# Performance work log

Hardware: AMD Instinct MI355X
Metric: run time of the kernel (lower is better)

The kernel has to match this reference:

```python
import jax, jax.numpy as jnp
import numpy as np

B, T, D = 4, 2048, 1024
GROUPS = 32
EPS = 1e-5
THETA = 10000.0


def _rope(x):
    # lucidrains RotaryEmbedding: interleaved pairs over the full dim
    d = x.shape[-1]
    t = x.shape[-2]
    inv_freq = 1.0 / (THETA ** (jnp.arange(0, d, 2, dtype=jnp.float32) / d))  # [d/2]
    freqs = jnp.arange(t, dtype=jnp.float32)[:, None] * inv_freq[None, :]      # [T, d/2]
    cos = jnp.cos(freqs).astype(x.dtype)
    sin = jnp.sin(freqs).astype(x.dtype)
    x1 = x[..., 0::2]
    x2 = x[..., 1::2]
    r1 = x1 * cos - x2 * sin
    r2 = x1 * sin + x2 * cos
    return jnp.stack([r1, r2], axis=-1).reshape(x.shape)


def _group_norm(z, weight, bias):
    # z: [N, C]; normalize per group of C//GROUPS channels
    n, c = z.shape
    zg = z.reshape(n, GROUPS, c // GROUPS)
    mean = zg.mean(axis=-1, keepdims=True)
    var = zg.var(axis=-1, keepdims=True)
    zg = (zg - mean) * jax.lax.rsqrt(var + EPS)
    return zg.reshape(n, c) * weight + bias


def setup_inputs() -> dict:
    key = jax.random.key(0)
    k1, k2, k3 = jax.random.split(key, 3)
    x = jax.random.normal(k1, (B, T, D), dtype=jnp.float32)
    W_in = jax.random.normal(k2, (D, 3 * D), dtype=jnp.float32) * (1.0 / np.sqrt(D))
    b_in = jax.random.normal(k3, (3 * D,), dtype=jnp.float32) * 0.02
    gn_weight = jnp.ones((D,), dtype=jnp.float32)
    gn_bias = jnp.zeros((D,), dtype=jnp.float32)
    return {"x": x, "W_in": W_in, "b_in": b_in, "gn_weight": gn_weight, "gn_bias": gn_bias}


def reference(x, W_in, b_in, gn_weight, gn_bias):
    b, t, c = x.shape
    qkv = x @ W_in + b_in                    # [B,T,3D]
    Q, K, V = jnp.split(qkv, 3, axis=-1)
    Q = jax.nn.relu(_rope(Q))
    K = jax.nn.relu(_rope(K))
    V = jax.nn.relu(V)
    A = jnp.einsum('btd,bsd->bts', Q, K)     # [B,T,T], no softmax
    y = jnp.einsum('bts,bsd->btd', A, V)     # [B,T,D]
    y = _group_norm(y.reshape(-1, c), gn_weight, gn_bias).reshape(b, t, c)
    # faithful to original: transpose(-2,-1).reshape(B,T,dim)
    return jnp.swapaxes(y, -2, -1).reshape(b, t, c)
```

## Files before the change

kernel.cpp:

```cpp
#include <hip/hip_runtime.h>


typedef unsigned short u16;
typedef __attribute__((ext_vector_type(8))) unsigned short u16x8;
typedef __attribute__((ext_vector_type(4))) float fx4;
typedef __attribute__((ext_vector_type(8))) __bf16 bfx8;

#define TP 129

__device__ __forceinline__ u16 f2bh(float v) {
  unsigned u = __float_as_uint(v);
  return (u16)((u + 0x7FFFu + ((u >> 16) & 1u)) >> 16);
}
__device__ __forceinline__ fx4 mfma16(bfx8 a, bfx8 b, fx4 c) {
  return __builtin_amdgcn_mfma_f32_16x16x32_bf16(a, b, c, 0, 0, 0);
}

__device__ __forceinline__ void gload16(const u16* g, u16* l) {
  __builtin_amdgcn_global_load_lds(
      (const __attribute__((address_space(1))) unsigned int*)(const void*)g,
      (__attribute__((address_space(3))) unsigned int*)(void*)l, 16, 0, 0);
}

__device__ __forceinline__ bfx8 ldsw(const u16* lds, int row, int slot) {
  const char* p = (const char*)lds + row * 128 + ((slot ^ (row & 7)) << 4);
  return __builtin_bit_cast(bfx8, *reinterpret_cast<const u16x8*>(p));
}

__device__ __forceinline__ void stage4(const u16* __restrict__ A,
                                       size_t rowBase, int stride, int k0,
                                       u16* lds, int w, int lane) {
#pragma unroll
  for (int i = 0; i < 4; ++i) {
    int c = ((w * 4 + i) << 6) + lane;
    int r = c >> 3, s = c & 7;
    int t = s ^ (r & 7);
    const u16* src = A + (rowBase + (size_t)r) * (size_t)stride + k0 + (t << 3);
    gload16(src, lds + ((w * 4 + i) << 9));
  }
}

__device__ inline void gemm_core_pipe(const u16* __restrict__ A, size_t aBase, int aStr,
                                      const u16* __restrict__ B, size_t bBase, int bStr, int K,
                                      u16* sA0, u16* sB0, u16* sA1, u16* sB1,
                                      fx4 acc[4][4], int w, int lane) {
  int wm = (w >> 1) * 64, wn = (w & 1) * 64;
  int lr = lane & 15, lk = lane >> 4;
  stage4(A, aBase, aStr, 0, sA0, w, lane);
  stage4(B, bBase, bStr, 0, sB0, w, lane);
  int NT = K >> 6;
  for (int t = 0; t < NT; ++t) {
    u16* cA = (t & 1) ? sA1 : sA0;
    u16* cB = (t & 1) ? sB1 : sB0;
    if (t + 1 < NT) {
      u16* nA = (t & 1) ? sA0 : sA1;
      u16* nB = (t & 1) ? sB0 : sB1;
      stage4(A, aBase, aStr, (t + 1) << 6, nA, w, lane);
      stage4(B, bBase, bStr, (t + 1) << 6, nB, w, lane);
      asm volatile("s_waitcnt vmcnt(8)" ::: "memory");
    } else {
      asm volatile("s_waitcnt vmcnt(0)" ::: "memory");
    }
    __builtin_amdgcn_s_barrier();
    __builtin_amdgcn_sched_barrier(0);
    bfx8 a[8], b[8];
#pragma unroll
    for (int h = 0; h < 2; ++h)
#pragma unroll
      for (int i = 0; i < 4; ++i) {
        a[h * 4 + i] = ldsw(cA, wm + i * 16 + lr, h * 4 + lk);
        b[h * 4 + i] = ldsw(cB, wn + i * 16 + lr, h * 4 + lk);
      }
    asm volatile("s_waitcnt lgkmcnt(0)" ::: "memory");
    __builtin_amdgcn_sched_barrier(0);
    __builtin_amdgcn_s_barrier();
#pragma unroll
    for (int h = 0; h < 2; ++h)
#pragma unroll
      for (int mi = 0; mi < 4; ++mi)
#pragma unroll
        for (int ni = 0; ni < 4; ++ni)
          acc[mi][ni] = mfma16(a[h * 4 + mi], b[h * 4 + ni], acc[mi][ni]);
  }
}

__global__ void k_ropetab(float2* __restrict__ tabTI, float2* __restrict__ tabIT) {
  int idx = blockIdx.x * 256 + threadIdx.x;
  int t, i;
  if (blockIdx.y == 0) {
    t = idx >> 9;
    i = idx & 511;
  } else {
    i = idx >> 11;
    t = idx & 2047;
  }
  float invf = exp2f(-(float)i * (13.287712379549449f / 512.f));
  float ang = (float)t * invf, s, c;
  sincosf(ang, &s, &c);
  if (blockIdx.y == 0)
    tabTI[idx] = make_float2(c, s);
  else
    tabIT[idx] = make_float2(c, s);
}

__global__ void k_transW(const float* __restrict__ W, u16* __restrict__ WTh) {
  __shared__ float tile[32][33];
  int n0 = blockIdx.x * 32, k0 = blockIdx.y * 32;
  int tid = threadIdx.x;
  int c = tid & 31, r4 = tid >> 5;
#pragma unroll
  for (int it = 0; it < 4; ++it) {
    int r = r4 + it * 8;
    tile[r][c] = W[(size_t)(k0 + r) * 3072 + n0 + c];
  }
  __syncthreads();
#pragma unroll
  for (int it = 0; it < 4; ++it) {
    int r = r4 + it * 8;
    WTh[(size_t)(n0 + r) * 1024 + k0 + c] = f2bh(tile[c][r]);
  }
}

__global__ void k_castX(const float* __restrict__ x, u16* __restrict__ xh) {
  size_t i = ((size_t)blockIdx.x * 256 + threadIdx.x) * 8;
  fx4 v0 = *reinterpret_cast<const fx4*>(x + i);
  fx4 v1 = *reinterpret_cast<const fx4*>(x + i + 4);
  u16x8 h;
#pragma unroll
  for (int j = 0; j < 4; ++j) {
    h[j] = f2bh(v0[j]);
    h[4 + j] = f2bh(v1[j]);
  }
  *reinterpret_cast<u16x8*>(xh + i) = h;
}

__global__ __launch_bounds__(256) void k_gemm1f(const u16* __restrict__ xh,
                                                const u16* __restrict__ WTh,
                                                const float* __restrict__ b_in,
                                                const float2* __restrict__ tabTI,
                                                const float2* __restrict__ tabIT,
                                                u16* __restrict__ Qh, u16* __restrict__ Kth,
                                                u16* __restrict__ Vth) {
  __shared__ __align__(16) float shbuf[128 * TP];
  u16* sA0 = (u16*)shbuf;
  u16* sB0 = sA0 + 128 * 64;
  u16* sA1 = sB0 + 128 * 64;
  u16* sB1 = sA1 + 128 * 64;
  int bid = blockIdx.x;
  int xcd = bid & 7, idx = bid >> 3;
  int mt = (xcd << 3) + (idx & 7), nt = idx >> 3;
  int m0 = mt << 7, n0 = nt << 7;
  int tid = threadIdx.x, lane = tid & 63, w = tid >> 6;
  int wm = (w >> 1) * 64, wn = (w & 1) * 64;
  int lr = lane & 15, lk = lane >> 4;
  fx4 acc[4][4];
#pragma unroll
  for (int i = 0; i < 4; ++i)
#pragma unroll
    for (int j = 0; j < 4; ++j) acc[i][j] = fx4{0.f, 0.f, 0.f, 0.f};

  gemm_core_pipe(xh, (size_t)m0, 1024, WTh, (size_t)n0, 1024, 1024,
                 sA0, sB0, sA1, sB1, acc, w, lane);

  float bv[4];
#pragma unroll
  for (int ni = 0; ni < 4; ++ni) bv[ni] = b_in[n0 + wn + ni * 16 + lr];
  __syncthreads();
#pragma unroll
  for (int mi = 0; mi < 4; ++mi)
#pragma unroll
    for (int ni = 0; ni < 4; ++ni)
#pragma unroll
      for (int r = 0; r < 4; ++r)
        shbuf[(wn + ni * 16 + lr) * TP + wm + mi * 16 + lk * 4 + r] = acc[mi][ni][r] + bv[ni];
  __syncthreads();

  int part = n0 >> 10;
  int d0 = n0 - (part << 10);
  int bb = m0 >> 11, tb = m0 & 2047;
  int rl0 = tid >> 4;
  int cc = (tid & 15) * 8;

  if (part == 2) {
#pragma unroll
    for (int pass = 0; pass < 8; ++pass) {
      int rl = rl0 + pass * 16;
      u16x8 o;
#pragma unroll
      for (int j = 0; j < 8; ++j) o[j] = f2bh(fmaxf(shbuf[rl * TP + cc + j], 0.f));
      *reinterpret_cast<u16x8*>(Vth + (((size_t)(bb << 10) + d0 + rl) << 11) + tb + cc) = o;
    }
  } else if (part == 1) {
#pragma unroll
    for (int pass = 0; pass < 8; ++pass) {
      int rl = rl0 + pass * 16;
      int d = d0 + rl;
      const float2* tp = tabIT + ((size_t)(d >> 1) << 11) + tb + cc;
      const float* e = shbuf + (rl & ~1) * TP + cc;
      const float* oo = shbuf + (rl | 1) * TP + cc;
      int isOdd = d & 1;
      u16x8 o;
#pragma unroll
      for (int j = 0; j < 8; ++j) {
        float2 cs = tp[j];
        float x1 = e[j], x2 = oo[j];
        float v = isOdd ? (x1 * cs.y + x2 * cs.x) : (x1 * cs.x - x2 * cs.y);
        o[j] = f2bh(fmaxf(v, 0.f));
      }
      *reinterpret_cast<u16x8*>(Kth + (((size_t)(bb << 10) + d) << 11) + tb + cc) = o;
    }
  } else {
#pragma unroll
    for (int pass = 0; pass < 8; ++pass) {
      int rl = rl0 + pass * 16;
      int m = m0 + rl, t = m & 2047;
      const float2* tp = tabTI + ((size_t)t << 9) + ((d0 + cc) >> 1);
      u16x8 o;
#pragma unroll
      for (int jp = 0; jp < 4; ++jp) {
        float x1 = shbuf[(cc + 2 * jp) * TP + rl];
        float x2 = shbuf[(cc + 2 * jp + 1) * TP + rl];
        float2 cs = tp[jp];
        o[2 * jp] = f2bh(fmaxf(x1 * cs.x - x2 * cs.y, 0.f));
        o[2 * jp + 1] = f2bh(fmaxf(x1 * cs.y + x2 * cs.x, 0.f));
      }
      *reinterpret_cast<u16x8*>(Qh + ((size_t)m << 10) + d0 + cc) = o;
    }
  }
}

__global__ __launch_bounds__(256) void k_gemm2(const u16* __restrict__ Kth, const u16* __restrict__ Vth,
                                               u16* __restrict__ KtVTh) {
  __shared__ u16 smem[4 * 128 * 64];
  u16* sA0 = smem;
  u16* sB0 = sA0 + 128 * 64;
  u16* sA1 = sB0 + 128 * 64;
  u16* sB1 = sA1 + 128 * 64;
  fx4 acc[4][4];
#pragma unroll
  for (int i = 0; i < 4; ++i)
#pragma unroll
    for (int j = 0; j < 4; ++j) acc[i][j] = fx4{0.f, 0.f, 0.f, 0.f};
  int b = blockIdx.z;
  int m0 = blockIdx.x << 7, n0 = blockIdx.y << 7;
  int tid = threadIdx.x, lane = tid & 63, w = tid >> 6;
  const u16* Ab = Kth + ((size_t)b << 21);
  const u16* Bb = Vth + ((size_t)b << 21);
  gemm_core_pipe(Ab, (size_t)m0, 2048, Bb, (size_t)n0, 2048, 2048,
                 sA0, sB0, sA1, sB1, acc, w, lane);
  int wm = (w >> 1) * 64, wn = (w & 1) * 64, lr = lane & 15, lk = lane >> 4;
#pragma unroll
  for (int mi = 0; mi < 4; ++mi)
#pragma unroll
    for (int ni = 0; ni < 4; ++ni)
#pragma unroll
      for (int r = 0; r < 4; ++r) {
        int m = m0 + wm + mi * 16 + lk * 4 + r;
        int n = n0 + wn + ni * 16 + lr;
        KtVTh[((size_t)b << 20) + ((size_t)n << 10) + m] = f2bh(acc[mi][ni][r]);
      }
}

__global__ __launch_bounds__(256) void k_gemm3g(const u16* __restrict__ Qh, const u16* __restrict__ KtVTh,
                                                const float* __restrict__ gw, const float* __restrict__ gb,
                                                float* __restrict__ out) {
  __shared__ u16 smem[4 * 128 * 64];
  u16* sA0 = smem;
  u16* sB0 = sA0 + 128 * 64;
  u16* sA1 = sB0 + 128 * 64;
  u16* sB1 = sA1 + 128 * 64;
  fx4 acc[4][4];
#pragma unroll
  for (int i = 0; i < 4; ++i)
#pragma unroll
    for (int j = 0; j < 4; ++j) acc[i][j] = fx4{0.f, 0.f, 0.f, 0.f};
  int b = blockIdx.z;
  int m0 = blockIdx.x << 7, n0 = blockIdx.y << 7;
  int tid = threadIdx.x, lane = tid & 63, w = tid >> 6;
  gemm_core_pipe(Qh, (size_t)(b * 2048 + m0), 1024, KtVTh + ((size_t)b << 20), (size_t)n0, 1024,
                 1024, sA0, sB0, sA1, sB1, acc, w, lane);
  int wm = (w >> 1) * 64, wn = (w & 1) * 64, lr = lane & 15, lk = lane >> 4;
  float wv[4], bvv[4];
#pragma unroll
  for (int ni = 0; ni < 4; ++ni) {
    int n = n0 + wn + ni * 16 + lr;
    wv[ni] = gw[n];
    bvv[ni] = gb[n];
  }
#pragma unroll
  for (int mi = 0; mi < 4; ++mi) {
    fx4 o0, o1, o2, o3;
#pragma unroll
    for (int r = 0; r < 4; ++r) {
      float v0 = acc[mi][0][r], v1 = acc[mi][1][r], v2 = acc[mi][2][r], v3 = acc[mi][3][r];
      float sA2 = v0 + v1, sB2 = v2 + v3;
#pragma unroll
      for (int mk = 1; mk <= 8; mk <<= 1) {
        sA2 += __shfl_xor(sA2, mk);
        sB2 += __shfl_xor(sB2, mk);
      }
      float mA = sA2 * (1.f / 32.f), mB = sB2 * (1.f / 32.f);
      float dA = (v0 - mA) * (v0 - mA) + (v1 - mA) * (v1 - mA);
      float dB = (v2 - mB) * (v2 - mB) + (v3 - mB) * (v3 - mB);
#pragma unroll
      for (int mk = 1; mk <= 8; mk <<= 1) {
        dA += __shfl_xor(dA, mk);
        dB += __shfl_xor(dB, mk);
      }
      float rA = rsqrtf(dA * (1.f / 32.f) + 1e-5f);
      float rB = rsqrtf(dB * (1.f / 32.f) + 1e-5f);
      o0[r] = (v0 - mA) * rA * wv[0] + bvv[0];
      o1[r] = (v1 - mA) * rA * wv[1] + bvv[1];
      o2[r] = (v2 - mB) * rB * wv[2] + bvv[2];
      o3[r] = (v3 - mB) * rB * wv[3] + bvv[3];
    }
    int mbase = m0 + wm + mi * 16 + lk * 4;
#pragma unroll
    for (int ni = 0; ni < 4; ++ni) {
      int n = n0 + wn + ni * 16 + lr;
      fx4 ov = (ni == 0) ? o0 : (ni == 1) ? o1 : (ni == 2) ? o2 : o3;
      *reinterpret_cast<fx4*>(out + (((size_t)(b << 10) + n) << 11) + mbase) = ov;
    }
  }
}

extern "C" void kernel_launch(void* const* d_in, const int* in_sizes, int n_in,
                              void* d_out, int out_size, void* d_ws, size_t ws_size,
                              hipStream_t stream) {
  const float* x = (const float*)d_in[0];
  const float* W = (const float*)d_in[1];
  const float* b_in = (const float*)d_in[2];
  const float* gnw = (const float*)d_in[3];
  const float* gnb = (const float*)d_in[4];
  float* out = (float*)d_out;
  char* ws = (char*)d_ws;

  u16* xh = (u16*)(ws + 0);
  u16* WTh = (u16*)(ws + 16777216);
  u16* Qh = (u16*)(ws + 23068672);
  u16* Kth = (u16*)(ws + 39845888);
  u16* Vth = (u16*)(ws + 56623104);
  u16* KtVTh = (u16*)(ws + 73400320);
  float2* tabTI = (float2*)(ws + 81788928);
  float2* tabIT = (float2*)(ws + 90177536);

  k_ropetab<<<dim3(4096, 2), 256, 0, stream>>>(tabTI, tabIT);
  k_transW<<<dim3(96, 32), 256, 0, stream>>>(W, WTh);
  k_castX<<<4096, 256, 0, stream>>>(x, xh);
  k_gemm1f<<<1536, 256, 0, stream>>>(xh, WTh, b_in, tabTI, tabIT, Qh, Kth, Vth);
  k_gemm2<<<dim3(8, 8, 4), 256, 0, stream>>>(Kth, Vth, KtVTh);
  k_gemm3g<<<dim3(16, 8, 4), 256, 0, stream>>>(Qh, KtVTh, gnw, gnb, out);
}
```

Baseline: 146.1 us.

## Switch GEMMs to 32x32x16 MFMA and merge prep kernels into one launch

Replaces the 16x16x32 bf16 MFMA tiles with 32x32x16 MFMA (2x2 f32x16 accumulators per wave) in all three GEMMs. The LDS fragment loads and every epilogue (bias/RoPE staging, KtV store, group-norm) are rewritten to match the new accumulator layout, with the KtV stores vectorised to 4-wide. The three preprocessing kernels (rope table, W transpose, x cast) are merged into one launch. The aim is fewer MFMA issues per K step, fewer LDS reads and less launch overhead. In exchange the group-norm reduction now needs more cross-lane shuffles.

Measured after the change: 155.0 us. +6.1%, slower.

```diff
diff --git a/kernel.cpp b/kernel.cpp
--- a/kernel.cpp
+++ b/kernel.cpp
@@ -2,8 +2,10 @@
 
 
 typedef unsigned short u16;
+typedef __attribute__((ext_vector_type(4))) unsigned short u16x4;
 typedef __attribute__((ext_vector_type(8))) unsigned short u16x8;
 typedef __attribute__((ext_vector_type(4))) float fx4;
+typedef __attribute__((ext_vector_type(16))) float f32x16;
 typedef __attribute__((ext_vector_type(8))) __bf16 bfx8;
 
 #define TP 129
@@ -12,8 +14,8 @@
   unsigned u = __float_as_uint(v);
   return (u16)((u + 0x7FFFu + ((u >> 16) & 1u)) >> 16);
 }
-__device__ __forceinline__ fx4 mfma16(bfx8 a, bfx8 b, fx4 c) {
-  return __builtin_amdgcn_mfma_f32_16x16x32_bf16(a, b, c, 0, 0, 0);
+__device__ __forceinline__ f32x16 mfma32(bfx8 a, bfx8 b, f32x16 c) {
+  return __builtin_amdgcn_mfma_f32_32x32x16_bf16(a, b, c, 0, 0, 0);
 }
 
 __device__ __forceinline__ void gload16(const u16* g, u16* l) {
@@ -43,9 +45,9 @@
 __device__ inline void gemm_core_pipe(const u16* __restrict__ A, size_t aBase, int aStr,
                                       const u16* __restrict__ B, size_t bBase, int bStr, int K,
                                       u16* sA0, u16* sB0, u16* sA1, u16* sB1,
-                                      fx4 acc[4][4], int w, int lane) {
+                                      f32x16 acc[2][2], int w, int lane) {
   int wm = (w >> 1) * 64, wn = (w & 1) * 64;
-  int lr = lane & 15, lk = lane >> 4;
+  int ln = lane & 31, hi = lane >> 5;
   stage4(A, aBase, aStr, 0, sA0, w, lane);
   stage4(B, bBase, bStr, 0, sB0, w, lane);
   int NT = K >> 6;
@@ -63,75 +65,77 @@
     }
     __builtin_amdgcn_s_barrier();
     __builtin_amdgcn_sched_barrier(0);
-    bfx8 a[8], b[8];
-#pragma unroll
-    for (int h = 0; h < 2; ++h)
-#pragma unroll
-      for (int i = 0; i < 4; ++i) {
-        a[h * 4 + i] = ldsw(cA, wm + i * 16 + lr, h * 4 + lk);
-        b[h * 4 + i] = ldsw(cB, wn + i * 16 + lr, h * 4 + lk);
+    bfx8 a[2][4], b[2][4];
+#pragma unroll
+    for (int rb = 0; rb < 2; ++rb)
+#pragma unroll
+      for (int ks = 0; ks < 4; ++ks) {
+        a[rb][ks] = ldsw(cA, wm + rb * 32 + ln, ks * 2 + hi);
+        b[rb][ks] = ldsw(cB, wn + rb * 32 + ln, ks * 2 + hi);
       }
     asm volatile("s_waitcnt lgkmcnt(0)" ::: "memory");
     __builtin_amdgcn_sched_barrier(0);
     __builtin_amdgcn_s_barrier();
 #pragma unroll
-    for (int h = 0; h < 2; ++h)
-#pragma unroll
-      for (int mi = 0; mi < 4; ++mi)
-#pragma unroll
-        for (int ni = 0; ni < 4; ++ni)
-          acc[mi][ni] = mfma16(a[h * 4 + mi], b[h * 4 + ni], acc[mi][ni]);
-  }
-}
-
-__global__ void k_ropetab(float2* __restrict__ tabTI, float2* __restrict__ tabIT) {
-  int idx = blockIdx.x * 256 + threadIdx.x;
-  int t, i;
-  if (blockIdx.y == 0) {
-    t = idx >> 9;
-    i = idx & 511;
+    for (int ks = 0; ks < 4; ++ks)
+#pragma unroll
+      for (int rb = 0; rb < 2; ++rb)
+#pragma unroll
+        for (int cb = 0; cb < 2; ++cb)
+          acc[rb][cb] = mfma32(a[rb][ks], b[cb][ks], acc[rb][cb]);
+  }
+}
+
+__global__ void k_prep(const float* __restrict__ x, const float* __restrict__ W,
+                       u16* __restrict__ xh, u16* __restrict__ WTh,
+                       float2* __restrict__ tabTI, float2* __restrict__ tabIT) {
+  __shared__ float tile[32][33];
+  int bid = blockIdx.x, tid = threadIdx.x;
+  if (bid < 4096) {
+    size_t i = ((size_t)bid * 256 + tid) * 8;
+    fx4 v0 = *reinterpret_cast<const fx4*>(x + i);
+    fx4 v1 = *reinterpret_cast<const fx4*>(x + i + 4);
+    u16x8 h;
+#pragma unroll
+    for (int j = 0; j < 4; ++j) {
+      h[j] = f2bh(v0[j]);
+      h[4 + j] = f2bh(v1[j]);
+    }
+    *reinterpret_cast<u16x8*>(xh + i) = h;
+  } else if (bid < 7168) {
+    int idx = bid - 4096;
+    int n0 = (idx % 96) * 32, k0 = (idx / 96) * 32;
+    int c = tid & 31, r4 = tid >> 5;
+#pragma unroll
+    for (int it = 0; it < 4; ++it) {
+      int r = r4 + it * 8;
+      tile[r][c] = W[(size_t)(k0 + r) * 3072 + n0 + c];
+    }
+    __syncthreads();
+#pragma unroll
+    for (int it = 0; it < 4; ++it) {
+      int r = r4 + it * 8;
+      WTh[(size_t)(n0 + r) * 1024 + k0 + c] = f2bh(tile[c][r]);
+    }
   } else {
-    i = idx >> 11;
-    t = idx & 2047;
-  }
-  float invf = exp2f(-(float)i * (13.287712379549449f / 512.f));
-  float ang = (float)t * invf, s, c;
-  sincosf(ang, &s, &c);
-  if (blockIdx.y == 0)
-    tabTI[idx] = make_float2(c, s);
-  else
-    tabIT[idx] = make_float2(c, s);
-}
-
-__global__ void k_transW(const float* __restrict__ W, u16* __restrict__ WTh) {
-  __shared__ float tile[32][33];
-  int n0 = blockIdx.x * 32, k0 = blockIdx.y * 32;
-  int tid = threadIdx.x;
-  int c = tid & 31, r4 = tid >> 5;
-#pragma unroll
-  for (int it = 0; it < 4; ++it) {
-    int r = r4 + it * 8;
-    tile[r][c] = W[(size_t)(k0 + r) * 3072 + n0 + c];
-  }
-  __syncthreads();
-#pragma unroll
-  for (int it = 0; it < 4; ++it) {
-    int r = r4 + it * 8;
-    WTh[(size_t)(n0 + r) * 1024 + k0 + c] = f2bh(tile[c][r]);
-  }
-}
-
-__global__ void k_castX(const float* __restrict__ x, u16* __restrict__ xh) {
-  size_t i = ((size_t)blockIdx.x * 256 + threadIdx.x) * 8;
-  fx4 v0 = *reinterpret_cast<const fx4*>(x + i);
-  fx4 v1 = *reinterpret_cast<const fx4*>(x + i + 4);
-  u16x8 h;
-#pragma unroll
-  for (int j = 0; j < 4; ++j) {
-    h[j] = f2bh(v0[j]);
-    h[4 + j] = f2bh(v1[j]);
-  }
-  *reinterpret_cast<u16x8*>(xh + i) = h;
+    int half = (bid - 7168) >> 12;
+    int idx = ((bid - 7168) & 4095) * 256 + tid;
+    int t, i;
+    if (half == 0) {
+      t = idx >> 9;
+      i = idx & 511;
+    } else {
+      i = idx >> 11;
+      t = idx & 2047;
+    }
+    float invf = exp2f(-(float)i * (13.287712379549449f / 512.f));
+    float ang = (float)t * invf, s, c;
+    sincosf(ang, &s, &c);
+    if (half == 0)
+      tabTI[idx] = make_float2(c, s);
+    else
+      tabIT[idx] = make_float2(c, s);
+  }
 }
 
 __global__ __launch_bounds__(256) void k_gemm1f(const u16* __restrict__ xh,
@@ -152,30 +156,34 @@
   int m0 = mt << 7, n0 = nt << 7;
   int tid = threadIdx.x, lane = tid & 63, w = tid >> 6;
   int wm = (w >> 1) * 64, wn = (w & 1) * 64;
-  int lr = lane & 15, lk = lane >> 4;
-  fx4 acc[4][4];
-#pragma unroll
-  for (int i = 0; i < 4; ++i)
-#pragma unroll
-    for (int j = 0; j < 4; ++j) acc[i][j] = fx4{0.f, 0.f, 0.f, 0.f};
+  int ln = lane & 31, hi = lane >> 5;
+  f32x16 acc[2][2];
+#pragma unroll
+  for (int i = 0; i < 2; ++i)
+#pragma unroll
+    for (int j = 0; j < 2; ++j) acc[i][j] = (f32x16)(0.f);
 
   gemm_core_pipe(xh, (size_t)m0, 1024, WTh, (size_t)n0, 1024, 1024,
                  sA0, sB0, sA1, sB1, acc, w, lane);
 
-  float bv[4];
-#pragma unroll
-  for (int ni = 0; ni < 4; ++ni) bv[ni] = b_in[n0 + wn + ni * 16 + lr];
+  int part = n0 >> 10;
+  float bv[2];
+#pragma unroll
+  for (int cb = 0; cb < 2; ++cb) bv[cb] = b_in[n0 + wn + cb * 32 + ln];
   __syncthreads();
 #pragma unroll
-  for (int mi = 0; mi < 4; ++mi)
-#pragma unroll
-    for (int ni = 0; ni < 4; ++ni)
-#pragma unroll
-      for (int r = 0; r < 4; ++r)
-        shbuf[(wn + ni * 16 + lr) * TP + wm + mi * 16 + lk * 4 + r] = acc[mi][ni][r] + bv[ni];
+  for (int rb = 0; rb < 2; ++rb)
+#pragma unroll
+    for (int cb = 0; cb < 2; ++cb)
+#pragma unroll
+      for (int e = 0; e < 16; ++e) {
+        float v = acc[rb][cb][e] + bv[cb];
+        int ml = wm + rb * 32 + (e & 3) + 8 * (e >> 2) + 4 * hi;
+        int nl = wn + cb * 32 + ln;
+        shbuf[nl * TP + ml] = v;
+      }
   __syncthreads();
 
-  int part = n0 >> 10;
   int d0 = n0 - (part << 10);
   int bb = m0 >> 11, tb = m0 & 2047;
   int rl0 = tid >> 4;
@@ -236,11 +244,11 @@
   u16* sB0 = sA0 + 128 * 64;
   u16* sA1 = sB0 + 128 * 64;
   u16* sB1 = sA1 + 128 * 64;
-  fx4 acc[4][4];
-#pragma unroll
-  for (int i = 0; i < 4; ++i)
-#pragma unroll
-    for (int j = 0; j < 4; ++j) acc[i][j] = fx4{0.f, 0.f, 0.f, 0.f};
+  f32x16 acc[2][2];
+#pragma unroll
+  for (int i = 0; i < 2; ++i)
+#pragma unroll
+    for (int j = 0; j < 2; ++j) acc[i][j] = (f32x16)(0.f);
   int b = blockIdx.z;
   int m0 = blockIdx.x << 7, n0 = blockIdx.y << 7;
   int tid = threadIdx.x, lane = tid & 63, w = tid >> 6;
@@ -248,16 +256,19 @@
   const u16* Bb = Vth + ((size_t)b << 21);
   gemm_core_pipe(Ab, (size_t)m0, 2048, Bb, (size_t)n0, 2048, 2048,
                  sA0, sB0, sA1, sB1, acc, w, lane);
-  int wm = (w >> 1) * 64, wn = (w & 1) * 64, lr = lane & 15, lk = lane >> 4;
-#pragma unroll
-  for (int mi = 0; mi < 4; ++mi)
-#pragma unroll
-    for (int ni = 0; ni < 4; ++ni)
-#pragma unroll
-      for (int r = 0; r < 4; ++r) {
-        int m = m0 + wm + mi * 16 + lk * 4 + r;
-        int n = n0 + wn + ni * 16 + lr;
-        KtVTh[((size_t)b << 20) + ((size_t)n << 10) + m] = f2bh(acc[mi][ni][r]);
+  int wm = (w >> 1) * 64, wn = (w & 1) * 64, ln = lane & 31, hi = lane >> 5;
+#pragma unroll
+  for (int rb = 0; rb < 2; ++rb)
+#pragma unroll
+    for (int cb = 0; cb < 2; ++cb)
+#pragma unroll
+      for (int q = 0; q < 4; ++q) {
+        u16x4 o;
+#pragma unroll
+        for (int j = 0; j < 4; ++j) o[j] = f2bh(acc[rb][cb][q * 4 + j]);
+        int m = m0 + wm + rb * 32 + q * 8 + hi * 4;
+        int n = n0 + wn + cb * 32 + ln;
+        *reinterpret_cast<u16x4*>(KtVTh + ((size_t)b << 20) + ((size_t)n << 10) + m) = o;
       }
 }
 
@@ -269,59 +280,52 @@
   u16* sB0 = sA0 + 128 * 64;
   u16* sA1 = sB0 + 128 * 64;
   u16* sB1 = sA1 + 128 * 64;
-  fx4 acc[4][4];
-#pragma unroll
-  for (int i = 0; i < 4; ++i)
-#pragma unroll
-    for (int j = 0; j < 4; ++j) acc[i][j] = fx4{0.f, 0.f, 0.f, 0.f};
+  f32x16 acc[2][2];
+#pragma unroll
+  for (int i = 0; i < 2; ++i)
+#pragma unroll
+    for (int j = 0; j < 2; ++j) acc[i][j] = (f32x16)(0.f);
   int b = blockIdx.z;
   int m0 = blockIdx.x << 7, n0 = blockIdx.y << 7;
   int tid = threadIdx.x, lane = tid & 63, w = tid >> 6;
   gemm_core_pipe(Qh, (size_t)(b * 2048 + m0), 1024, KtVTh + ((size_t)b << 20), (size_t)n0, 1024,
                  1024, sA0, sB0, sA1, sB1, acc, w, lane);
-  int wm = (w >> 1) * 64, wn = (w & 1) * 64, lr = lane & 15, lk = lane >> 4;
-  float wv[4], bvv[4];
-#pragma unroll
-  for (int ni = 0; ni < 4; ++ni) {
-    int n = n0 + wn + ni * 16 + lr;
-    wv[ni] = gw[n];
-    bvv[ni] = gb[n];
-  }
-#pragma unroll
-  for (int mi = 0; mi < 4; ++mi) {
-    fx4 o0, o1, o2, o3;
-#pragma unroll
-    for (int r = 0; r < 4; ++r) {
-      float v0 = acc[mi][0][r], v1 = acc[mi][1][r], v2 = acc[mi][2][r], v3 = acc[mi][3][r];
-      float sA2 = v0 + v1, sB2 = v2 + v3;
-#pragma unroll
-      for (int mk = 1; mk <= 8; mk <<= 1) {
-        sA2 += __shfl_xor(sA2, mk);
-        sB2 += __shfl_xor(sB2, mk);
-      }
-      float mA = sA2 * (1.f / 32.f), mB = sB2 * (1.f / 32.f);
-      float dA = (v0 - mA) * (v0 - mA) + (v1 - mA) * (v1 - mA);
-      float dB = (v2 - mB) * (v2 - mB) + (v3 - mB) * (v3 - mB);
-#pragma unroll
-      for (int mk = 1; mk <= 8; mk <<= 1) {
-        dA += __shfl_xor(dA, mk);
-        dB += __shfl_xor(dB, mk);
-      }
-      float rA = rsqrtf(dA * (1.f / 32.f) + 1e-5f);
-      float rB = rsqrtf(dB * (1.f / 32.f) + 1e-5f);
-      o0[r] = (v0 - mA) * rA * wv[0] + bvv[0];
-      o1[r] = (v1 - mA) * rA * wv[1] + bvv[1];
-      o2[r] = (v2 - mB) * rB * wv[2] + bvv[2];
-      o3[r] = (v3 - mB) * rB * wv[3] + bvv[3];
-    }
-    int mbase = m0 + wm + mi * 16 + lk * 4;
-#pragma unroll
-    for (int ni = 0; ni < 4; ++ni) {
-      int n = n0 + wn + ni * 16 + lr;
-      fx4 ov = (ni == 0) ? o0 : (ni == 1) ? o1 : (ni == 2) ? o2 : o3;
-      *reinterpret_cast<fx4*>(out + (((size_t)(b << 10) + n) << 11) + mbase) = ov;
-    }
-  }
+  int wm = (w >> 1) * 64, wn = (w & 1) * 64, ln = lane & 31, hi = lane >> 5;
+  float wv[2], bvv[2];
+#pragma unroll
+  for (int cb = 0; cb < 2; ++cb) {
+    int n = n0 + wn + cb * 32 + ln;
+    wv[cb] = gw[n];
+    bvv[cb] = gb[n];
+  }
+#pragma unroll
+  for (int rb = 0; rb < 2; ++rb)
+#pragma unroll
+    for (int cb = 0; cb < 2; ++cb) {
+      float o[16];
+#pragma unroll
+      for (int e = 0; e < 16; ++e) {
+        float v = acc[rb][cb][e];
+        float s = v;
+#pragma unroll
+        for (int mk = 1; mk <= 16; mk <<= 1) s += __shfl_xor(s, mk);
+        float mean = s * (1.f / 32.f);
+        float d = (v - mean) * (v - mean);
+#pragma unroll
+        for (int mk = 1; mk <= 16; mk <<= 1) d += __shfl_xor(d, mk);
+        float rstd = rsqrtf(d * (1.f / 32.f) + 1e-5f);
+        o[e] = (v - mean) * rstd * wv[cb] + bvv[cb];
+      }
+      int n = n0 + wn + cb * 32 + ln;
+#pragma unroll
+      for (int q = 0; q < 4; ++q) {
+        fx4 ov;
+#pragma unroll
+        for (int j = 0; j < 4; ++j) ov[j] = o[q * 4 + j];
+        int m = m0 + wm + rb * 32 + q * 8 + hi * 4;
+        *reinterpret_cast<fx4*>(out + (((size_t)(b << 10) + n) << 11) + m) = ov;
+      }
+    }
 }
 
 extern "C" void kernel_launch(void* const* d_in, const int* in_sizes, int n_in,
@@ -344,9 +348,7 @@
   float2* tabTI = (float2*)(ws + 81788928);
   float2* tabIT = (float2*)(ws + 90177536);
 
-  k_ropetab<<<dim3(4096, 2), 256, 0, stream>>>(tabTI, tabIT);
-  k_transW<<<dim3(96, 32), 256, 0, stream>>>(W, WTh);
-  k_castX<<<4096, 256, 0, stream>>>(x, xh);
+  k_prep<<<15360, 256, 0, stream>>>(x, W, xh, WTh, tabTI, tabIT);
   k_gemm1f<<<1536, 256, 0, stream>>>(xh, WTh, b_in, tabTI, tabIT, Qh, Kth, Vth);
   k_gemm2<<<dim3(8, 8, 4), 256, 0, stream>>>(Kth, Vth, KtVTh);
   k_gemm3g<<<dim3(16, 8, 4), 256, 0, stream>>>(Qh, KtVTh, gnw, gnb, out);
```
